# Optimization experiments

Hardware: AMD Instinct MI355X
Metric: run time of the kernel (lower is better)

## Reference

```python
import jax, jax.numpy as jnp
import numpy as np
from jax import lax
import math

B, L, D = 2, 1024, 1024
H = 16
HD = D // H
DS = 16            # d_state
EXP = 2
DIN = EXP * D      # d_inner = 2048
DCONV = 4
DTR = math.ceil(D / 16)  # dt_rank = 64
EPS = 1e-5


def setup_inputs() -> dict:
    key = jax.random.key(0)
    ks = jax.random.split(key, 24)
    g = lambda i, shape, s=0.02: (jax.random.normal(ks[i], shape, dtype=jnp.float32) * s)
    A_log = jnp.log(jnp.tile(jnp.arange(1, DS + 1, dtype=jnp.float32)[None, :], (DIN, 1)))
    return {
        "x": jax.random.normal(ks[0], (B, L, D), dtype=jnp.float32),
        # MambaWrapper pre-norm
        "mnorm_w": jnp.ones((D,), jnp.float32), "mnorm_b": jnp.zeros((D,), jnp.float32),
        # MambaBlock params
        "in_proj_w": g(1, (2 * DIN, D)),
        "conv_w": g(2, (DIN, 1, DCONV), 0.1), "conv_b": jnp.zeros((DIN,), jnp.float32),
        "x_proj_w": g(3, (DTR + 2 * DS, DIN)),
        "dt_proj_w": g(4, (DIN, DTR)), "dt_proj_b": g(5, (DIN,), 0.01),
        "A_log": A_log, "D_skip": jnp.ones((DIN,), jnp.float32),
        "out_proj_w": g(6, (D, DIN)),
        # attention branch
        "norm1_w": jnp.ones((D,), jnp.float32), "norm1_b": jnp.zeros((D,), jnp.float32),
        "wqkv_w": g(7, (D + 2 * HD, D)), "wqkv_b": jnp.zeros((D + 2 * HD,), jnp.float32),
        "oattn_w": g(8, (D, D)), "oattn_b": jnp.zeros((D,), jnp.float32),
        # parallel fusion: Linear(2D->D) + LayerNorm
        "fuse_w": g(9, (D, 2 * D)), "fuse_b": jnp.zeros((D,), jnp.float32),
        "fln_w": jnp.ones((D,), jnp.float32), "fln_b": jnp.zeros((D,), jnp.float32),
    }


def _ln(x, w, b):
    m = x.mean(-1, keepdims=True)
    xc = x - m
    v = (xc * xc).mean(-1, keepdims=True)
    return xc * lax.rsqrt(v + EPS) * w + b


def _selective_scan(u, delta, A, Bm, Cm, D_skip):
    # u, delta: (b,l,din); A: (din,n); Bm,Cm: (b,l,n)
    dA = jnp.exp(delta[..., None] * A)                    # (b,l,din,n)
    dBu = delta[..., None] * Bm[:, :, None, :] * u[..., None]

    def step(h, inp):
        dA_t, dBu_t, C_t = inp                            # (b,din,n),(b,din,n),(b,n)
        h = dA_t * h + dBu_t
        y = jnp.einsum('bdn,bn->bd', h, C_t)
        return h, y

    h0 = jnp.zeros((u.shape[0], u.shape[2], A.shape[1]), u.dtype)
    _, ys = lax.scan(step, h0, (dA.transpose(1, 0, 2, 3), dBu.transpose(1, 0, 2, 3), Cm.transpose(1, 0, 2)))
    return ys.transpose(1, 0, 2) + u * D_skip             # (b,l,din)


def _mamba_branch(x, mnorm_w, mnorm_b, in_proj_w, conv_w, conv_b, x_proj_w,
                  dt_proj_w, dt_proj_b, A_log, D_skip, out_proj_w):
    xn = _ln(x, mnorm_w, mnorm_b)
    xr = xn @ in_proj_w.T                                 # (b,l,2*din)
    u, res = xr[..., :DIN], xr[..., DIN:]
    # depthwise causal conv1d (torch pads d_conv-1 both sides then slices [:l])
    uc = u.transpose(0, 2, 1)                             # (b,din,l)
    uc = lax.conv_general_dilated(uc, conv_w, (1,), [(DCONV - 1, 0)],
                                  dimension_numbers=('NCH', 'OIH', 'NCH'),
                                  feature_group_count=DIN) + conv_b[None, :, None]
    u = jax.nn.silu(uc.transpose(0, 2, 1))
    dbc = u @ x_proj_w.T                                  # (b,l,dtr+2n)
    delta = jax.nn.softplus(dbc[..., :DTR] @ dt_proj_w.T + dt_proj_b)
    Bm = dbc[..., DTR:DTR + DS]
    Cm = dbc[..., DTR + DS:]
    y = _selective_scan(u, delta, -jnp.exp(A_log), Bm, Cm, D_skip)
    y = y * jax.nn.silu(res)
    return (y @ out_proj_w.T) + x                         # dropout=identity (eval), +residual


def _mqa_branch(x, norm1_w, norm1_b, wqkv_w, wqkv_b, oattn_w, oattn_b):
    xn = _ln(x, norm1_w, norm1_b)
    qkv = xn @ wqkv_w.T + wqkv_b
    q = qkv[..., :D].reshape(B, L, H, HD)
    k = qkv[..., D:D + HD]                                # shared single K head (b,l,hd)
    v = qkv[..., D + HD:]
    scores = jnp.einsum('blhd,bsd->bhls', q, k) / math.sqrt(HD)
    causal = jnp.tril(jnp.ones((L, L), bool))
    scores = jnp.where(causal, scores, jnp.finfo(scores.dtype).min)
    attn = jax.nn.softmax(scores, axis=-1)
    o = jnp.einsum('bhls,bsd->blhd', attn, v).reshape(B, L, D)
    return x + (o @ oattn_w.T + oattn_b)


def reference(x, mnorm_w, mnorm_b, in_proj_w, conv_w, conv_b, x_proj_w,
              dt_proj_w, dt_proj_b, A_log, D_skip, out_proj_w,
              norm1_w, norm1_b, wqkv_w, wqkv_b, oattn_w, oattn_b,
              fuse_w, fuse_b, fln_w, fln_b):
    mamba_out = _mamba_branch(x, mnorm_w, mnorm_b, in_proj_w, conv_w, conv_b, x_proj_w,
                              dt_proj_w, dt_proj_b, A_log, D_skip, out_proj_w)
    attn_out = _mqa_branch(x, norm1_w, norm1_b, wqkv_w, wqkv_b, oattn_w, oattn_b)
    combined = jnp.concatenate([mamba_out, attn_out], axis=-1)
    fused = _ln(combined @ fuse_w.T + fuse_b, fln_w, fln_b)
    return fused
```

## Files before the change

kernel.cpp:

```cpp
#include <hip/hip_runtime.h>
#include <hip/hip_bf16.h>
#include <hip/hip_fp16.h>
#include <cstddef>


using bf16 = __hip_bfloat16;
using frag8 = __attribute__((ext_vector_type(8))) short;
using f32x4 = __attribute__((ext_vector_type(4))) float;

__device__ __forceinline__ float siluf(float x) { return x / (1.f + __expf(-x)); }

__device__ __forceinline__ int sigmode(const unsigned int* sig) {
    const unsigned int s = *sig;
    return s == 0x3F800000u ? 1 : (s == 0x3C003C00u ? 2 : 0);
}
__device__ __forceinline__ float ldx(const void* p, size_t i, int m) {
    if (m == 1) return reinterpret_cast<const float*>(p)[i];
    if (m == 2) return __half2float(reinterpret_cast<const __half*>(p)[i]);
    return __bfloat162float(reinterpret_cast<const bf16*>(p)[i]);
}

__device__ __forceinline__ void gload_lds16(const void* g, void* l) {
    __builtin_amdgcn_global_load_lds(
        (const __attribute__((address_space(1))) unsigned int*)g,
        (__attribute__((address_space(3))) unsigned int*)l, 16, 0, 0);
}

__global__ void sentinel_kernel(float* out, float code) {
    if (threadIdx.x == 0) out[0] = code;
}

__global__ __launch_bounds__(256) void wconv_kernel(const void* __restrict__ W, size_t off,
                                                    bf16* __restrict__ dst, int total8,
                                                    const unsigned int* __restrict__ sig) {
    const int g = blockIdx.x * 256 + threadIdx.x;
    if (g >= total8) return;
    const int md = sigmode(sig);
    const size_t i0 = off + (size_t)g * 8;
    union { bf16 h[8]; uint4 v; } u;
    if (md == 0) {
        u.v = *reinterpret_cast<const uint4*>((const bf16*)W + i0);
    } else {
#pragma unroll
        for (int j = 0; j < 8; ++j) u.h[j] = __float2bfloat16(ldx(W, i0 + j, md));
    }
    *reinterpret_cast<uint4*>(dst + (size_t)g * 8) = u.v;
}

__global__ __launch_bounds__(256) void wconv2_kernel(
    const void* __restrict__ W1, bf16* __restrict__ dst1, int total8_1,
    const void* __restrict__ W2, bf16* __restrict__ dst2, int total8_2,
    const unsigned int* __restrict__ sig) {
    const int g = blockIdx.x * 256 + threadIdx.x;
    const int md = sigmode(sig);
    const void* W;
    bf16* dst;
    int gg;
    if (g < total8_1) { W = W1; dst = dst1; gg = g; }
    else if (g < total8_1 + total8_2) { W = W2; dst = dst2; gg = g - total8_1; }
    else return;
    const size_t i0 = (size_t)gg * 8;
    union { bf16 h[8]; uint4 v; } u;
    if (md == 0) {
        u.v = *reinterpret_cast<const uint4*>((const bf16*)W + i0);
    } else {
#pragma unroll
        for (int j = 0; j < 8; ++j) u.h[j] = __float2bfloat16(ldx(W, i0 + j, md));
    }
    *reinterpret_cast<uint4*>(dst + i0) = u.v;
}

template <typename TO>
__global__ __launch_bounds__(256) void ln_kernel(
    const void* __restrict__ x, int x_from_in,
    const void* __restrict__ w, const void* __restrict__ b,
    const unsigned int* __restrict__ sig, TO* __restrict__ out) {
    const int md = sigmode(sig);
    const int xm = x_from_in ? md : 0;
    const int row = blockIdx.x;
    const int tid = threadIdx.x;
    __shared__ float red[256];
    const size_t base = (size_t)row * 1024;
    float v[4];
    float s = 0.f;
#pragma unroll
    for (int i = 0; i < 4; ++i) { v[i] = ldx(x, base + tid + i * 256, xm); s += v[i]; }
    red[tid] = s;
    __syncthreads();
    for (int st = 128; st > 0; st >>= 1) {
        if (tid < st) red[tid] += red[tid + st];
        __syncthreads();
    }
    const float mean = red[0] * (1.f / 1024.f);
    __syncthreads();
    float s2 = 0.f;
#pragma unroll
    for (int i = 0; i < 4; ++i) { v[i] -= mean; s2 += v[i] * v[i]; }
    red[tid] = s2;
    __syncthreads();
    for (int st = 128; st > 0; st >>= 1) {
        if (tid < st) red[tid] += red[tid + st];
        __syncthreads();
    }
    const float inv = rsqrtf(red[0] * (1.f / 1024.f) + 1e-5f);
#pragma unroll
    for (int i = 0; i < 4; ++i) {
        const int d = tid + i * 256;
        const float r = v[i] * inv * ldx(w, d, md) + ldx(b, d, md);
        if constexpr (sizeof(TO) == 4) out[base + d] = r;
        else out[base + d] = __float2bfloat16(r);
    }
}

template <int BM, int BN>
__global__ __launch_bounds__(256) void mfma_gemm(
    const bf16* __restrict__ A1, const bf16* __restrict__ A2, int KA1, int lda,
    const bf16* __restrict__ Wb,
    const void* __restrict__ bias,
    const void* __restrict__ resid, int ldr,
    bf16* __restrict__ C, int ldc,
    int K, int Nbound, int act, const unsigned int* __restrict__ sig,
    bf16* __restrict__ vt) {
    constexpr int NFR = (BN == 64) ? 1 : ((BM == 128) ? 4 : 2);
    const int md = sigmode(sig);
    __shared__ __align__(16) bf16 Als[BM * 32];
    __shared__ __align__(16) bf16 Wls[BN * 32];
    const int tid = threadIdx.x;
    const int lane = tid & 63;
    const int w = tid >> 6;
    const int arow = (BM == 128) ? ((w >> 1) * 64) : 0;
    const int bcol = (BN == 64) ? (w * 16) : ((BM == 128) ? ((w & 1) * 64) : (w * 32));
    const int m0 = blockIdx.y * BM;
    const int n0 = blockIdx.x * BN;
    f32x4 acc[4][NFR];
#pragma unroll
    for (int i = 0; i < 4; ++i)
#pragma unroll
        for (int j = 0; j < NFR; ++j) acc[i][j] = {0.f, 0.f, 0.f, 0.f};
    const int fm = lane & 15;
    const int fq = lane >> 4;
    for (int kk = 0; kk < K; kk += 32) {
        if constexpr (BM == 128) {
#pragma unroll
            for (int i = 0; i < 2; ++i) {
                const int chunk = i * 256 + tid;
                const int r = chunk >> 2, q = chunk & 3;
                const int gk = kk + q * 8;
                const bf16* srcA = (A2 != nullptr && gk >= KA1)
                    ? (A2 + (size_t)(m0 + r) * lda + (gk - KA1))
                    : (A1 + (size_t)(m0 + r) * lda + gk);
                gload_lds16(srcA, (char*)Als + (size_t)(i * 256 + w * 64) * 16);
            }
        } else {
            const int r = tid >> 2, q = tid & 3;
            const int gk = kk + q * 8;
            const bf16* srcA = (A2 != nullptr && gk >= KA1)
                ? (A2 + (size_t)(m0 + r) * lda + (gk - KA1))
                : (A1 + (size_t)(m0 + r) * lda + gk);
            gload_lds16(srcA, (char*)Als + (size_t)(w * 64) * 16);
        }
#pragma unroll
        for (int i = 0; i < (BN == 64 ? 1 : 2); ++i) {
            const int chunk = i * 256 + tid;
            const int r = chunk >> 2, q = chunk & 3;
            const bf16* srcW = Wb + (size_t)(n0 + r) * K + kk + q * 8;
            gload_lds16(srcW, (char*)Wls + (size_t)(i * 256 + w * 64) * 16);
        }
        __syncthreads();
        frag8 af[4], bfr[NFR];
#pragma unroll
        for (int ms = 0; ms < 4; ++ms)
            af[ms] = *reinterpret_cast<const frag8*>(&Als[(size_t)(arow + ms * 16 + fm) * 32 + fq * 8]);
#pragma unroll
        for (int ns = 0; ns < NFR; ++ns)
            bfr[ns] = *reinterpret_cast<const frag8*>(&Wls[(size_t)(bcol + ns * 16 + fm) * 32 + fq * 8]);
#pragma unroll
        for (int ms = 0; ms < 4; ++ms)
#pragma unroll
            for (int ns = 0; ns < NFR; ++ns)
                acc[ms][ns] = __builtin_amdgcn_mfma_f32_16x16x32_bf16(af[ms], bfr[ns], acc[ms][ns], 0, 0, 0);
        __syncthreads();
    }
#pragma unroll
    for (int ms = 0; ms < 4; ++ms) {
#pragma unroll
        for (int r = 0; r < 4; ++r) {
            const int m = m0 + arow + ms * 16 + fq * 4 + r;
#pragma unroll
            for (int ns = 0; ns < NFR; ++ns) {
                const int n = n0 + bcol + ns * 16 + fm;
                if (n < Nbound) {
                    float v = acc[ms][ns][r];
                    if (bias) v += ldx(bias, n, md);
                    if (resid) v += ldx(resid, (size_t)m * ldr + n, md);
                    if (act == 1) v = (v > 20.f) ? v : log1pf(expf(v));
                    const bf16 hv = __float2bfloat16(v);
                    C[(size_t)m * ldc + n] = hv;
                    if (vt != nullptr && n >= 1088) {
                        vt[((size_t)((m >> 10) * 64 + (n - 1088))) * 1024 + (m & 1023)] = hv;
                    }
                }
            }
        }
    }
}

__global__ __launch_bounds__(256) void conv_silu_kernel(
    const bf16* __restrict__ u0, int us, const void* __restrict__ cw,
    const void* __restrict__ cb, const unsigned int* __restrict__ sig,
    bf16* __restrict__ u) {
    const int md = sigmode(sig);
    const int idx = blockIdx.x * 256 + threadIdx.x;
    const int c8 = (idx & 255) * 8;
    const int bl = idx >> 8;
    const int l = bl & 1023;
    float acc[8];
#pragma unroll
    for (int i = 0; i < 8; ++i) acc[i] = ldx(cb, c8 + i, md);
#pragma unroll
    for (int k = 0; k < 4; ++k) {
        const int ls = l - 3 + k;
        if (ls >= 0) {
            union { frag8 v; bf16 h[8]; } uin;
            uin.v = *reinterpret_cast<const frag8*>(u0 + (size_t)(bl - 3 + k) * us + c8);
#pragma unroll
            for (int i = 0; i < 8; ++i)
                acc[i] += __bfloat162float(uin.h[i]) * ldx(cw, (c8 + i) * 4 + k, md);
        }
    }
    union { frag8 v; bf16 h[8]; } uo;
#pragma unroll
    for (int i = 0; i < 8; ++i) uo.h[i] = __float2bfloat16(siluf(acc[i]));
    *reinterpret_cast<frag8*>(u + (size_t)bl * 2048 + c8) = uo.v;
}

__global__ __launch_bounds__(512) void scan_kernel(
    bf16* __restrict__ delta_y, const bf16* __restrict__ u,
    const bf16* __restrict__ dbc, const bf16* __restrict__ res,
    const void* __restrict__ A_log, const void* __restrict__ D_skip,
    const unsigned int* __restrict__ sig) {
    constexpr int DYS = 4096;
    constexpr int US  = 2048;
    constexpr int BS  = 96;
    constexpr int PRS = 20;
    constexpr int PJS = 168;
    const int md = sigmode(sig);
    const int n = threadIdx.x & 15;
    const int j = threadIdx.x >> 4;
    const int bx = blockIdx.x;
    const int c = ((bx & 7) << 8) | (bx >> 3);
    const int b = blockIdx.y;
    __shared__ float Ac[32 * 17], Hc[32 * 17], h0s[32 * 17];
    __shared__ __align__(16) float P[32 * PJS];
    __shared__ __align__(16) bf16 Dcol[1024], Ucol[1024];
    const float acoef = -expf(ldx(A_log, c * 16 + n, md));
    const float dsk = ldx(D_skip, c, md);
    const int t0 = j * 32;
    const int bt0 = b * 1024 + t0;

    {
        const int tid = threadIdx.x;
#pragma unroll
        for (int rr = 0; rr < 2; ++rr) {
            const int t = tid + rr * 512;
            Dcol[t] = delta_y[(size_t)(b * 1024 + t) * DYS + c];
            Ucol[t] = u[(size_t)(b * 1024 + t) * US + c];
        }
    }
    __syncthreads();

    {
        const bf16* pb = dbc + (size_t)bt0 * BS + 64 + n;
        float hloc = 0.f, aprod = 1.f;
#pragma unroll 8
        for (int tt = 0; tt < 32; ++tt) {
            const float dlt = __bfloat162float(Dcol[t0 + tt]);
            const float ut = __bfloat162float(Ucol[t0 + tt]);
            const float Bn = __bfloat162float(*pb);
            const float a = __expf(dlt * acoef);
            hloc = a * hloc + dlt * Bn * ut;
            aprod *= a;
            pb += BS;
        }
        Ac[j * 17 + n] = aprod;
        Hc[j * 17 + n] = hloc;
    }
    __syncthreads();
    if (threadIdx.x < 16) {
        float e = 0.f;
        for (int jj = 0; jj < 32; ++jj) {
            h0s[jj * 17 + threadIdx.x] = e;
            e = Ac[jj * 17 + threadIdx.x] * e + Hc[jj * 17 + threadIdx.x];
        }
    }
    __syncthreads();

    float h = h0s[j * 17 + n];
    float psum[2];
    float* Pj = &P[j * PJS];
    {
        const bf16* pb = dbc + (size_t)bt0 * BS + 64 + n;
        const int nq = n >> 3;
        const int nr = n & 7;
#pragma unroll
        for (int q = 0; q < 4; ++q) {
#pragma unroll
            for (int k = 0; k < 8; ++k) {
                const int tt = q * 8 + k;
                const float dlt = __bfloat162float(Dcol[t0 + tt]);
                const float ut = __bfloat162float(Ucol[t0 + tt]);
                const float Bn = __bfloat162float(pb[0]);
                const float Cn = __bfloat162float(pb[16]);
                const float a = __expf(dlt * acoef);
                h = a * h + dlt * Bn * ut;
                Pj[k * PRS + n] = h * Cn;
                pb += BS;
            }
            if (nq == (q & 1)) {
                const f32x4* pr = reinterpret_cast<const f32x4*>(&Pj[nr * PRS]);
                float s = 0.f;
#pragma unroll
                for (int v = 0; v < 4; ++v) {
                    const f32x4 q4 = pr[v];
                    s += q4[0] + q4[1] + q4[2] + q4[3];
                }
                psum[q >> 1] = s;
            }
        }
    }
#pragma unroll
    for (int half = 0; half < 2; ++half) {
        const int tl = t0 + half * 16 + n;
        const size_t id = (size_t)(b * 1024 + tl) * DYS + c;
        const float ut = __bfloat162float(Ucol[tl]);
        const float r = __bfloat162float(res[id]);
        delta_y[id] = __float2bfloat16((psum[half] + ut * dsk) * siluf(r));
    }
}

__global__ __launch_bounds__(256) void attn_mfma(const bf16* __restrict__ qkv,
                                                 const bf16* __restrict__ Vt,
                                                 bf16* __restrict__ o) {
    const int tid = threadIdx.x;
    const int lane = tid & 63;
    const int wv = tid >> 6;
    const int fm = lane & 15, quad = lane >> 4;
    const int qt = blockIdx.x, h = blockIdx.y, b = blockIdx.z;
    __shared__ __align__(16) char shbuf[4 * 64 * 72 * sizeof(bf16)];
    bf16 (*Pls)[64][72] = reinterpret_cast<bf16 (*)[64][72]>(shbuf);
    float (*Ols)[64][68] = reinterpret_cast<float (*)[64][68]>(shbuf);
    __shared__ float Mst[2][64], Lst[2][64];

    frag8 qf[4][2];
#pragma unroll
    for (int ms = 0; ms < 4; ++ms)
#pragma unroll
        for (int kq = 0; kq < 2; ++kq)
            qf[ms][kq] = *reinterpret_cast<const frag8*>(
                qkv + ((size_t)(b * 1024 + qt * 64 + ms * 16 + fm)) * 1152 + h * 64 + kq * 32 + quad * 8);

    float mrun[4][4], lrun[4][4];
    f32x4 acco[4][4];
#pragma unroll
    for (int ms = 0; ms < 4; ++ms)
#pragma unroll
        for (int r = 0; r < 4; ++r) { mrun[ms][r] = -1.0e30f; lrun[ms][r] = 0.f; }
#pragma unroll
    for (int ms = 0; ms < 4; ++ms)
#pragma unroll
        for (int nd = 0; nd < 4; ++nd) acco[ms][nd] = {0.f, 0.f, 0.f, 0.f};

    for (int st = wv; st <= qt; st += 4) {
        f32x4 accs[4][4];
#pragma unroll
        for (int ms = 0; ms < 4; ++ms)
#pragma unroll
            for (int ns = 0; ns < 4; ++ns) accs[ms][ns] = {0.f, 0.f, 0.f, 0.f};
        __builtin_amdgcn_s_setprio(1);
#pragma unroll
        for (int ns = 0; ns < 4; ++ns) {
            frag8 kf[2];
#pragma unroll
            for (int kq = 0; kq < 2; ++kq)
                kf[kq] = *reinterpret_cast<const frag8*>(
                    qkv + ((size_t)(b * 1024 + st * 64 + ns * 16 + fm)) * 1152 + 1024 + kq * 32 + quad * 8);
#pragma unroll
            for (int ms = 0; ms < 4; ++ms) {
                accs[ms][ns] = __builtin_amdgcn_mfma_f32_16x16x32_bf16(qf[ms][0], kf[0], accs[ms][ns], 0, 0, 0);
                accs[ms][ns] = __builtin_amdgcn_mfma_f32_16x16x32_bf16(qf[ms][1], kf[1], accs[ms][ns], 0, 0, 0);
            }
        }
        __builtin_amdgcn_s_setprio(0);
        const bool diag = (st == qt);
#pragma unroll
        for (int ms = 0; ms < 4; ++ms) {
            float alpha[4];
#pragma unroll
            for (int r = 0; r < 4; ++r) {
                const int ql = ms * 16 + quad * 4 + r;
                float sv[4];
#pragma unroll
                for (int ns = 0; ns < 4; ++ns) {
                    const int sl = ns * 16 + fm;
                    sv[ns] = (!diag || sl <= ql) ? accs[ms][ns][r] * 0.125f : -1.0e30f;
                }
                float mloc = fmaxf(fmaxf(sv[0], sv[1]), fmaxf(sv[2], sv[3]));
                mloc = fmaxf(mloc, __shfl_xor(mloc, 1));
                mloc = fmaxf(mloc, __shfl_xor(mloc, 2));
                mloc = fmaxf(mloc, __shfl_xor(mloc, 4));
                mloc = fmaxf(mloc, __shfl_xor(mloc, 8));
                const float mnew = fmaxf(mrun[ms][r], mloc);
                alpha[r] = __expf(mrun[ms][r] - mnew);
                float rs = 0.f;
#pragma unroll
                for (int ns = 0; ns < 4; ++ns) {
                    const float p = __expf(sv[ns] - mnew);
                    rs += p;
                    Pls[wv][ms * 16 + quad * 4 + r][ns * 16 + fm] = __float2bfloat16(p);
                }
                rs += __shfl_xor(rs, 1);
                rs += __shfl_xor(rs, 2);
                rs += __shfl_xor(rs, 4);
                rs += __shfl_xor(rs, 8);
                lrun[ms][r] = lrun[ms][r] * alpha[r] + rs;
                mrun[ms][r] = mnew;
            }
#pragma unroll
            for (int nd = 0; nd < 4; ++nd)
#pragma unroll
                for (int r = 0; r < 4; ++r) acco[ms][nd][r] *= alpha[r];
        }
        frag8 pf[4][2];
#pragma unroll
        for (int ms = 0; ms < 4; ++ms)
#pragma unroll
            for (int ks = 0; ks < 2; ++ks)
                pf[ms][ks] = *reinterpret_cast<const frag8*>(&Pls[wv][ms * 16 + fm][ks * 32 + quad * 8]);
        __builtin_amdgcn_s_setprio(1);
#pragma unroll
        for (int nd = 0; nd < 4; ++nd) {
            frag8 vf[2];
#pragma unroll
            for (int ks = 0; ks < 2; ++ks)
                vf[ks] = *reinterpret_cast<const frag8*>(
                    Vt + ((size_t)b * 64 + nd * 16 + fm) * 1024 + st * 64 + ks * 32 + quad * 8);
#pragma unroll
            for (int ms = 0; ms < 4; ++ms) {
                acco[ms][nd] = __builtin_amdgcn_mfma_f32_16x16x32_bf16(pf[ms][0], vf[0], acco[ms][nd], 0, 0, 0);
                acco[ms][nd] = __builtin_amdgcn_mfma_f32_16x16x32_bf16(pf[ms][1], vf[1], acco[ms][nd], 0, 0, 0);
            }
        }
        __builtin_amdgcn_s_setprio(0);
    }

    __syncthreads();
    if (wv >= 2) {
        const int s = wv - 2;
#pragma unroll
        for (int ms = 0; ms < 4; ++ms)
#pragma unroll
            for (int r = 0; r < 4; ++r) {
                const int q = ms * 16 + quad * 4 + r;
                Mst[s][q] = mrun[ms][r];
                Lst[s][q] = lrun[ms][r];
#pragma unroll
                for (int nd = 0; nd < 4; ++nd)
                    Ols[s][q][nd * 16 + fm] = acco[ms][nd][r];
            }
    }
    __syncthreads();
    if (wv < 2) {
#pragma unroll
        for (int ms = 0; ms < 4; ++ms)
#pragma unroll
            for (int r = 0; r < 4; ++r) {
                const int q = ms * 16 + quad * 4 + r;
                const float m1 = Mst[wv][q], l1 = Lst[wv][q];
                const float M = fmaxf(mrun[ms][r], m1);
                const float a0 = __expf(mrun[ms][r] - M);
                const float a1 = __expf(m1 - M);
                lrun[ms][r] = lrun[ms][r] * a0 + l1 * a1;
                mrun[ms][r] = M;
#pragma unroll
                for (int nd = 0; nd < 4; ++nd)
                    acco[ms][nd][r] = acco[ms][nd][r] * a0 + Ols[wv][q][nd * 16 + fm] * a1;
            }
    }
    __syncthreads();
    if (wv == 1) {
#pragma unroll
        for (int ms = 0; ms < 4; ++ms)
#pragma unroll
            for (int r = 0; r < 4; ++r) {
                const int q = ms * 16 + quad * 4 + r;
                Mst[0][q] = mrun[ms][r];
                Lst[0][q] = lrun[ms][r];
#pragma unroll
                for (int nd = 0; nd < 4; ++nd)
                    Ols[0][q][nd * 16 + fm] = acco[ms][nd][r];
            }
    }
    __syncthreads();
    if (wv == 0) {
#pragma unroll
        for (int ms = 0; ms < 4; ++ms)
#pragma unroll
            for (int r = 0; r < 4; ++r) {
                const int q = ms * 16 + quad * 4 + r;
                const float m1 = Mst[0][q], l1 = Lst[0][q];
                const float M = fmaxf(mrun[ms][r], m1);
                const float a0 = __expf(mrun[ms][r] - M);
                const float a1 = __expf(m1 - M);
                const float L = lrun[ms][r] * a0 + l1 * a1;
                const float inv = 1.f / fmaxf(L, 1e-30f);
                const size_t row = (size_t)(b * 1024 + qt * 64 + q);
#pragma unroll
                for (int nd = 0; nd < 4; ++nd)
                    o[row * 1024 + h * 64 + nd * 16 + fm] =
                        __float2bfloat16((acco[ms][nd][r] * a0 + Ols[0][q][nd * 16 + fm] * a1) * inv);
            }
    }
}

extern "C" void kernel_launch(void* const* d_in, const int* in_sizes, int n_in,
                              void* d_out, int out_size, void* d_ws, size_t ws_size,
                              hipStream_t stream) {
    float* out = (float*)d_out;

    static const int kExp[22] = {
        2097152, 1024, 1024, 4194304, 8192, 2048, 196608, 131072, 2048, 32768,
        2048, 2097152, 1024, 1024, 1179648, 1152, 1048576, 1024, 2097152, 1024,
        1024, 1024};
    const size_t kNeedBytes = 29360128;
    float code = 0.f;
    if (n_in != 22) code = 65536.f * (32 + (n_in & 31));
    else if (out_size != 2097152) code = 65536.f * 200.f;
    else {
        for (int i = 0; i < 22; ++i)
            if (in_sizes[i] != kExp[i]) { code = 65536.f * (64 + i); break; }
        if (code == 0.f && ws_size < kNeedBytes)
            code = 65536.f * (128.f + (float)(ws_size >> 20));
    }
    if (code != 0.f) {
        sentinel_kernel<<<dim3(1), dim3(64), 0, stream>>>(out, code);
        return;
    }

    const unsigned int* sig = (const unsigned int*)d_in[1];

    bf16* ws = (bf16*)d_ws;
    bf16* Aslot = ws;
    bf16* Bslot = ws + 2097152;
    bf16* Cslot = ws + 6291456;
    bf16* Dslot = ws + 10485760;
    bf16* dbc    = Aslot;
    bf16* xprojW = Aslot + 262144;
    bf16* dtW    = Aslot + 524288;
    bf16* u0res  = Bslot;
    bf16* mambaOut = Dslot;
    bf16* DsHi = Dslot + 2097152;
    bf16* BsHi = Bslot + 2097152;
    bf16* Vt   = Bslot + 1572864;

    const dim3 b256(256);
    const int NOSPLIT = 1 << 30;
    const int NB = 1 << 30;

    ln_kernel<bf16><<<dim3(2048), b256, 0, stream>>>(d_in[0], 1, d_in[1], d_in[2], sig, Aslot);
    wconv_kernel<<<dim3(2048), b256, 0, stream>>>(d_in[3], 0, Dslot, 524288, sig);
    mfma_gemm<128, 128><<<dim3(32, 16), b256, 0, stream>>>(Aslot, nullptr, NOSPLIT, 1024,
        Dslot, nullptr, nullptr, 0, u0res, 4096, 1024, NB, 0, sig, nullptr);
    conv_silu_kernel<<<dim3(2048), b256, 0, stream>>>(u0res, 4096, d_in[4], d_in[5], sig, Dslot);
    wconv2_kernel<<<dim3(160), b256, 0, stream>>>(d_in[6], xprojW, 24576, d_in[7], dtW, 16384, sig);
    mfma_gemm<64, 128><<<dim3(1, 32), b256, 0, stream>>>(Dslot, nullptr, NOSPLIT, 2048,
        xprojW, nullptr, nullptr, 0, dbc, 96, 2048, 96, 0, sig, nullptr);
    mfma_gemm<64, 128><<<dim3(16, 32), b256, 0, stream>>>(dbc, nullptr, NOSPLIT, 96,
        dtW, d_in[8], nullptr, 0, u0res, 4096, 64, NB, 1, sig, nullptr);
    scan_kernel<<<dim3(2048, 2), dim3(512), 0, stream>>>(u0res, Dslot, dbc, u0res + 2048,
        d_in[9], d_in[10], sig);
    wconv_kernel<<<dim3(1024), b256, 0, stream>>>(d_in[11], 0, DsHi, 262144, sig);
    mfma_gemm<64, 64><<<dim3(16, 32), b256, 0, stream>>>(u0res, nullptr, NOSPLIT, 4096,
        DsHi, nullptr, d_in[0], 1024, mambaOut, 1024, 2048, NB, 0, sig, nullptr);

    ln_kernel<bf16><<<dim3(2048), b256, 0, stream>>>(d_in[0], 1, d_in[12], d_in[13], sig, Aslot);
    wconv_kernel<<<dim3(576), b256, 0, stream>>>(d_in[14], 0, Bslot, 147456, sig);
    mfma_gemm<64, 64><<<dim3(18, 32), b256, 0, stream>>>(Aslot, nullptr, NOSPLIT, 1024,
        Bslot, d_in[15], nullptr, 0, Cslot, 1152, 1024, NB, 0, sig, Vt);
    attn_mfma<<<dim3(16, 16, 2), dim3(256), 0, stream>>>(Cslot, Vt, DsHi);
    wconv_kernel<<<dim3(512), b256, 0, stream>>>(d_in[16], 0, Bslot, 131072, sig);
    mfma_gemm<64, 64><<<dim3(16, 32), b256, 0, stream>>>(DsHi, nullptr, NOSPLIT, 1024,
        Bslot, d_in[17], d_in[0], 1024, BsHi, 1024, 1024, NB, 0, sig, nullptr);

    wconv_kernel<<<dim3(1024), b256, 0, stream>>>(d_in[18], 0, Cslot, 262144, sig);
    mfma_gemm<64, 64><<<dim3(16, 32), b256, 0, stream>>>(mambaOut, BsHi, 1024, 1024,
        Cslot, d_in[19], nullptr, 0, Aslot, 1024, 2048, NB, 0, sig, nullptr);
    ln_kernel<float><<<dim3(2048), b256, 0, stream>>>(Aslot, 0, d_in[20], d_in[21], sig, out);
}
```

Before: 596.9 us.

## Fold weight-conversion kernels into neighbouring kernels and use wave-shuffle LayerNorm reductions

Removes five separate weight bf16-conversion launches by appending extra blocks to the LayerNorm, conv/SiLU, scan and attention kernels, so each conversion runs inside a kernel that was already launched. LayerNorm switches from a 256-entry shared-memory tree reduction to wave shuffles plus a four-value shared combine, which cuts barriers. The aim is to reduce launch count and synchronization overhead. The extra blocks may delay or imbalance the host kernels, and the scan and attention conversion blocks must not write buffers those kernels read; in the attention kernel the write goes to Bslot while it reads Cslot, Vt and DsHi.

```diff
diff --git a/kernel.cpp b/kernel.cpp
--- a/kernel.cpp
+++ b/kernel.cpp
@@ -28,6 +28,19 @@
 
 __global__ void sentinel_kernel(float* out, float code) {
     if (threadIdx.x == 0) out[0] = code;
+}
+
+__device__ __forceinline__ void wconv_body(const void* __restrict__ W, size_t off,
+                                           bf16* __restrict__ dst, int g, int md) {
+    const size_t i0 = off + (size_t)g * 8;
+    union { bf16 h[8]; uint4 v; } u;
+    if (md == 0) {
+        u.v = *reinterpret_cast<const uint4*>((const bf16*)W + i0);
+    } else {
+#pragma unroll
+        for (int j = 0; j < 8; ++j) u.h[j] = __float2bfloat16(ldx(W, i0 + j, md));
+    }
+    *reinterpret_cast<uint4*>(dst + (size_t)g * 8) = u.v;
 }
 
 __global__ __launch_bounds__(256) void wconv_kernel(const void* __restrict__ W, size_t off,
@@ -35,80 +48,60 @@
                                                     const unsigned int* __restrict__ sig) {
     const int g = blockIdx.x * 256 + threadIdx.x;
     if (g >= total8) return;
-    const int md = sigmode(sig);
-    const size_t i0 = off + (size_t)g * 8;
-    union { bf16 h[8]; uint4 v; } u;
-    if (md == 0) {
-        u.v = *reinterpret_cast<const uint4*>((const bf16*)W + i0);
-    } else {
-#pragma unroll
-        for (int j = 0; j < 8; ++j) u.h[j] = __float2bfloat16(ldx(W, i0 + j, md));
-    }
-    *reinterpret_cast<uint4*>(dst + (size_t)g * 8) = u.v;
-}
-
-__global__ __launch_bounds__(256) void wconv2_kernel(
-    const void* __restrict__ W1, bf16* __restrict__ dst1, int total8_1,
-    const void* __restrict__ W2, bf16* __restrict__ dst2, int total8_2,
-    const unsigned int* __restrict__ sig) {
-    const int g = blockIdx.x * 256 + threadIdx.x;
-    const int md = sigmode(sig);
-    const void* W;
-    bf16* dst;
-    int gg;
-    if (g < total8_1) { W = W1; dst = dst1; gg = g; }
-    else if (g < total8_1 + total8_2) { W = W2; dst = dst2; gg = g - total8_1; }
-    else return;
-    const size_t i0 = (size_t)gg * 8;
-    union { bf16 h[8]; uint4 v; } u;
-    if (md == 0) {
-        u.v = *reinterpret_cast<const uint4*>((const bf16*)W + i0);
-    } else {
-#pragma unroll
-        for (int j = 0; j < 8; ++j) u.h[j] = __float2bfloat16(ldx(W, i0 + j, md));
-    }
-    *reinterpret_cast<uint4*>(dst + i0) = u.v;
-}
-
+    wconv_body(W, off, dst, g, sigmode(sig));
+}
+
+__device__ __forceinline__ float waveSum(float v) {
+    v += __shfl_xor(v, 1);  v += __shfl_xor(v, 2);  v += __shfl_xor(v, 4);
+    v += __shfl_xor(v, 8);  v += __shfl_xor(v, 16); v += __shfl_xor(v, 32);
+    return v;
+}
 template <typename TO>
-__global__ __launch_bounds__(256) void ln_kernel(
-    const void* __restrict__ x, int x_from_in,
+__device__ __forceinline__ void ln_body(
+    const void* __restrict__ x, int xm,
     const void* __restrict__ w, const void* __restrict__ b,
-    const unsigned int* __restrict__ sig, TO* __restrict__ out) {
-    const int md = sigmode(sig);
-    const int xm = x_from_in ? md : 0;
-    const int row = blockIdx.x;
-    const int tid = threadIdx.x;
-    __shared__ float red[256];
+    int md, TO* __restrict__ out, int row, int tid) {
+    __shared__ float wred[4];
+    const int lane = tid & 63, wv = tid >> 6;
     const size_t base = (size_t)row * 1024;
     float v[4];
     float s = 0.f;
 #pragma unroll
     for (int i = 0; i < 4; ++i) { v[i] = ldx(x, base + tid + i * 256, xm); s += v[i]; }
-    red[tid] = s;
-    __syncthreads();
-    for (int st = 128; st > 0; st >>= 1) {
-        if (tid < st) red[tid] += red[tid + st];
-        __syncthreads();
-    }
-    const float mean = red[0] * (1.f / 1024.f);
-    __syncthreads();
+    s = waveSum(s);
+    if (lane == 0) wred[wv] = s;
+    __syncthreads();
+    const float mean = (wred[0] + wred[1] + wred[2] + wred[3]) * (1.f / 1024.f);
     float s2 = 0.f;
 #pragma unroll
     for (int i = 0; i < 4; ++i) { v[i] -= mean; s2 += v[i] * v[i]; }
-    red[tid] = s2;
-    __syncthreads();
-    for (int st = 128; st > 0; st >>= 1) {
-        if (tid < st) red[tid] += red[tid + st];
-        __syncthreads();
-    }
-    const float inv = rsqrtf(red[0] * (1.f / 1024.f) + 1e-5f);
+    s2 = waveSum(s2);
+    __syncthreads();
+    if (lane == 0) wred[wv] = s2;
+    __syncthreads();
+    const float inv = rsqrtf((wred[0] + wred[1] + wred[2] + wred[3]) * (1.f / 1024.f) + 1e-5f);
 #pragma unroll
     for (int i = 0; i < 4; ++i) {
         const int d = tid + i * 256;
         const float r = v[i] * inv * ldx(w, d, md) + ldx(b, d, md);
         if constexpr (sizeof(TO) == 4) out[base + d] = r;
         else out[base + d] = __float2bfloat16(r);
+    }
+}
+
+template <typename TO>
+__global__ __launch_bounds__(256) void ln_wconv_kernel(
+    const void* __restrict__ x, int x_from_in,
+    const void* __restrict__ w, const void* __restrict__ b,
+    const unsigned int* __restrict__ sig, TO* __restrict__ out, int lnB,
+    const void* __restrict__ W, bf16* __restrict__ dst, int total8) {
+    const int md = sigmode(sig);
+    const int bx = blockIdx.x;
+    if (bx < lnB) {
+        ln_body<TO>(x, x_from_in ? md : 0, w, b, md, out, bx, threadIdx.x);
+    } else {
+        const int g = (bx - lnB) * 256 + threadIdx.x;
+        if (g < total8) wconv_body(W, 0, dst, g, md);
     }
 }
 
@@ -205,12 +198,21 @@
     }
 }
 
-__global__ __launch_bounds__(256) void conv_silu_kernel(
+__global__ __launch_bounds__(256) void conv_wconv_kernel(
     const bf16* __restrict__ u0, int us, const void* __restrict__ cw,
     const void* __restrict__ cb, const unsigned int* __restrict__ sig,
-    bf16* __restrict__ u) {
+    bf16* __restrict__ u,
+    const void* __restrict__ W1, bf16* __restrict__ dst1, int t1,
+    const void* __restrict__ W2, bf16* __restrict__ dst2, int t2) {
     const int md = sigmode(sig);
-    const int idx = blockIdx.x * 256 + threadIdx.x;
+    const int bx = blockIdx.x;
+    if (bx >= 2048) {
+        const int g = (bx - 2048) * 256 + threadIdx.x;
+        if (g < t1) wconv_body(W1, 0, dst1, g, md);
+        else if (g < t1 + t2) wconv_body(W2, 0, dst2, g - t1, md);
+        return;
+    }
+    const int idx = bx * 256 + threadIdx.x;
     const int c8 = (idx & 255) * 8;
     const int bl = idx >> 8;
     const int l = bl & 1023;
@@ -238,16 +240,21 @@
     bf16* __restrict__ delta_y, const bf16* __restrict__ u,
     const bf16* __restrict__ dbc, const bf16* __restrict__ res,
     const void* __restrict__ A_log, const void* __restrict__ D_skip,
-    const unsigned int* __restrict__ sig) {
+    const unsigned int* __restrict__ sig,
+    const void* __restrict__ Wop, bf16* __restrict__ dstOp) {
     constexpr int DYS = 4096;
     constexpr int US  = 2048;
     constexpr int BS  = 96;
     constexpr int PRS = 20;
     constexpr int PJS = 168;
     const int md = sigmode(sig);
+    const int bx = blockIdx.x;
+    if (blockIdx.y == 2) {
+        if (bx < 512) wconv_body(Wop, 0, dstOp, bx * 512 + threadIdx.x, md);
+        return;
+    }
     const int n = threadIdx.x & 15;
     const int j = threadIdx.x >> 4;
-    const int bx = blockIdx.x;
     const int c = ((bx & 7) << 8) | (bx >> 3);
     const int b = blockIdx.y;
     __shared__ float Ac[32 * 17], Hc[32 * 17], h0s[32 * 17];
@@ -340,8 +347,21 @@
 
 __global__ __launch_bounds__(256) void attn_mfma(const bf16* __restrict__ qkv,
                                                  const bf16* __restrict__ Vt,
-                                                 bf16* __restrict__ o) {
+                                                 bf16* __restrict__ o,
+                                                 const void* __restrict__ Woa,
+                                                 bf16* __restrict__ dstOa,
+                                                 const unsigned int* __restrict__ sig) {
     const int tid = threadIdx.x;
+    if (blockIdx.z == 2) {
+        const int md = sigmode(sig);
+        const int bid = blockIdx.y * 16 + blockIdx.x;
+#pragma unroll
+        for (int it = 0; it < 2; ++it) {
+            const int g = bid * 256 + tid + it * 65536;
+            wconv_body(Woa, 0, dstOa, g, md);
+        }
+        return;
+    }
     const int lane = tid & 63;
     const int wv = tid >> 6;
     const int fm = lane & 15, quad = lane >> 4;
@@ -566,33 +586,32 @@
     const int NOSPLIT = 1 << 30;
     const int NB = 1 << 30;
 
-    ln_kernel<bf16><<<dim3(2048), b256, 0, stream>>>(d_in[0], 1, d_in[1], d_in[2], sig, Aslot);
-    wconv_kernel<<<dim3(2048), b256, 0, stream>>>(d_in[3], 0, Dslot, 524288, sig);
+    ln_wconv_kernel<bf16><<<dim3(4096), b256, 0, stream>>>(
+        d_in[0], 1, d_in[1], d_in[2], sig, Aslot, 2048, d_in[3], Dslot, 524288);
     mfma_gemm<128, 128><<<dim3(32, 16), b256, 0, stream>>>(Aslot, nullptr, NOSPLIT, 1024,
         Dslot, nullptr, nullptr, 0, u0res, 4096, 1024, NB, 0, sig, nullptr);
-    conv_silu_kernel<<<dim3(2048), b256, 0, stream>>>(u0res, 4096, d_in[4], d_in[5], sig, Dslot);
-    wconv2_kernel<<<dim3(160), b256, 0, stream>>>(d_in[6], xprojW, 24576, d_in[7], dtW, 16384, sig);
+    conv_wconv_kernel<<<dim3(2208), b256, 0, stream>>>(u0res, 4096, d_in[4], d_in[5], sig,
+        Dslot, d_in[6], xprojW, 24576, d_in[7], dtW, 16384);
     mfma_gemm<64, 128><<<dim3(1, 32), b256, 0, stream>>>(Dslot, nullptr, NOSPLIT, 2048,
         xprojW, nullptr, nullptr, 0, dbc, 96, 2048, 96, 0, sig, nullptr);
     mfma_gemm<64, 128><<<dim3(16, 32), b256, 0, stream>>>(dbc, nullptr, NOSPLIT, 96,
         dtW, d_in[8], nullptr, 0, u0res, 4096, 64, NB, 1, sig, nullptr);
-    scan_kernel<<<dim3(2048, 2), dim3(512), 0, stream>>>(u0res, Dslot, dbc, u0res + 2048,
-        d_in[9], d_in[10], sig);
-    wconv_kernel<<<dim3(1024), b256, 0, stream>>>(d_in[11], 0, DsHi, 262144, sig);
+    scan_kernel<<<dim3(2048, 3), dim3(512), 0, stream>>>(u0res, Dslot, dbc, u0res + 2048,
+        d_in[9], d_in[10], sig, d_in[11], DsHi);
     mfma_gemm<64, 64><<<dim3(16, 32), b256, 0, stream>>>(u0res, nullptr, NOSPLIT, 4096,
         DsHi, nullptr, d_in[0], 1024, mambaOut, 1024, 2048, NB, 0, sig, nullptr);
 
-    ln_kernel<bf16><<<dim3(2048), b256, 0, stream>>>(d_in[0], 1, d_in[12], d_in[13], sig, Aslot);
-    wconv_kernel<<<dim3(576), b256, 0, stream>>>(d_in[14], 0, Bslot, 147456, sig);
+    ln_wconv_kernel<bf16><<<dim3(2624), b256, 0, stream>>>(
+        d_in[0], 1, d_in[12], d_in[13], sig, Aslot, 2048, d_in[14], Bslot, 147456);
     mfma_gemm<64, 64><<<dim3(18, 32), b256, 0, stream>>>(Aslot, nullptr, NOSPLIT, 1024,
         Bslot, d_in[15], nullptr, 0, Cslot, 1152, 1024, NB, 0, sig, Vt);
-    attn_mfma<<<dim3(16, 16, 2), dim3(256), 0, stream>>>(Cslot, Vt, DsHi);
-    wconv_kernel<<<dim3(512), b256, 0, stream>>>(d_in[16], 0, Bslot, 131072, sig);
+    attn_mfma<<<dim3(16, 16, 3), b256, 0, stream>>>(Cslot, Vt, DsHi, d_in[16], Bslot, sig);
     mfma_gemm<64, 64><<<dim3(16, 32), b256, 0, stream>>>(DsHi, nullptr, NOSPLIT, 1024,
         Bslot, d_in[17], d_in[0], 1024, BsHi, 1024, 1024, NB, 0, sig, nullptr);
 
     wconv_kernel<<<dim3(1024), b256, 0, stream>>>(d_in[18], 0, Cslot, 262144, sig);
     mfma_gemm<64, 64><<<dim3(16, 32), b256, 0, stream>>>(mambaOut, BsHi, 1024, 1024,
         Cslot, d_in[19], nullptr, 0, Aslot, 1024, 2048, NB, 0, sig, nullptr);
-    ln_kernel<float><<<dim3(2048), b256, 0, stream>>>(Aslot, 0, d_in[20], d_in[21], sig, out);
-}
+    ln_wconv_kernel<float><<<dim3(2048), b256, 0, stream>>>(
+        Aslot, 0, d_in[20], d_in[21], sig, out, 2048, nullptr, nullptr, 0);
+}
```

Result: slower. 731.4 us (+22.5%).
